# Optimization experiments

Measured on AMD Instinct MI355X. Metric: run time of the kernel, lower is better.

Reference implementation:

```python
import jax, jax.numpy as jnp
import numpy as np

# --- model constants (from init_kwargs) ---
COUNT = 8          # number of layer stacks (king buckets)
L1 = 3072          # input feature dim (2*L1//2 == L1)
L2 = 15            # first hidden dim per stack (l1 outputs L2+1: L2 hidden + 1 skip)
L3 = 32            # second hidden dim per stack
SQ_CORR = 127.0 / 128.0   # sqcrele_correction_factor
MAX_ACT = 1.0             # max_hidden_activation (clipped ReLU ceiling)
BATCH = 32768


def setup_inputs() -> dict:
    key = jax.random.key(0)
    ks = jax.random.split(key, 8)
    x = jax.random.normal(ks[0], (BATCH, L1), dtype=jnp.float32)
    routing_data = jax.random.randint(ks[1], (BATCH,), 0, COUNT, dtype=jnp.int64)
    # StackedLinear weights: [count, out_features, in_features]
    w1 = jax.random.normal(ks[2], (COUNT, L2 + 1, L1), dtype=jnp.float32) * 0.01
    b1 = jax.random.normal(ks[3], (COUNT, L2 + 1), dtype=jnp.float32) * 0.01
    w2 = jax.random.normal(ks[4], (COUNT, L3, 2 * L2), dtype=jnp.float32) * 0.05
    b2 = jax.random.normal(ks[5], (COUNT, L3), dtype=jnp.float32) * 0.01
    w3 = jax.random.normal(ks[6], (COUNT, 1, L3), dtype=jnp.float32) * 0.05
    b3 = jnp.zeros((COUNT, 1), dtype=jnp.float32)  # output bias zeroed in __init__
    return {"x": x, "routing_data": routing_data,
            "w1": w1, "b1": b1, "w2": w2, "b2": b2, "w3": w3, "b3": b3}


def reference(x, routing_data, w1, b1, w2, b2, w3, b3):
    # l1: apply all COUNT linears to the shared input -> [B, count, L2+1]
    l1c = jnp.einsum('bi,coi->bco', x, w1) + b1
    l1x, l1x_out = l1c[..., :L2], l1c[..., L2:]            # [B,c,L2], [B,c,1]
    sqr_l1x = (l1x * l1x) * SQ_CORR
    h1 = jnp.clip(jnp.concatenate([sqr_l1x, l1x], axis=2), 0.0, MAX_ACT)  # [B,c,2*L2]
    # l2: per-stack linear -> [B, count, L3]
    h2 = jnp.clip(jnp.einsum('bci,coi->bco', h1, w2) + b2, 0.0, MAX_ACT)
    # output: per-stack linear -> [B, count, 1], plus skip connection
    l3x = jnp.einsum('bci,coi->bco', h2, w3) + b3 + l1x_out
    # hard-index routing: gather the selected stack per batch element -> [B, 1]
    idx = routing_data.astype(jnp.int32)[:, None, None]
    return jnp.take_along_axis(l3x, idx, axis=1).squeeze(1)
```

## Files before the change

### kernel.cpp

```cpp
#include <hip/hip_runtime.h>

#define NEXP   8
#define L1DIM  3072
#define BATCH  32768
#define SQCORR (127.0f / 128.0f)
#define CHUNK  256
#define NCHUNK (L1DIM / CHUNK)

#define CUR_STRIDE  16
#define WS_CURSORS  0
#define WS_SORTED   (NEXP * CUR_STRIDE)
#define NBLK_SORT   (BATCH / 256)
#define BLK_PER_E   (BATCH / 16)
#define NBLK_MAIN   (NEXP * BLK_PER_E)

__global__ void init_k(int* ws) {
    if (threadIdx.x < NEXP)
        ws[WS_CURSORS + threadIdx.x * CUR_STRIDE] = threadIdx.x * BATCH;
}

__global__ void scatter_k(const int* __restrict__ routing, int* ws) {
    __shared__ int h[NEXP];
    __shared__ int base[NEXP];
    if (threadIdx.x < NEXP) h[threadIdx.x] = 0;
    __syncthreads();
    int i = blockIdx.x * 256 + threadIdx.x;
    int e = routing[i];
    int rank = atomicAdd(&h[e], 1);
    __syncthreads();
    if (threadIdx.x < NEXP)
        base[threadIdx.x] =
            atomicAdd(&ws[WS_CURSORS + threadIdx.x * CUR_STRIDE], h[threadIdx.x]);
    __syncthreads();
    ws[WS_SORTED + base[e] + rank] = i;
}

__device__ __forceinline__ void lds_cp16(void* lds, const void* g) {
    __builtin_amdgcn_global_load_lds(
        (const __attribute__((address_space(1))) void*)g,
        (__attribute__((address_space(3))) void*)lds, 16, 0, 0);
}

__global__ __launch_bounds__(256, 3) void moe_main_k(
        const float* __restrict__ x, const int* __restrict__ ws,
        const float* __restrict__ w1, const float* __restrict__ b1,
        const float* __restrict__ w2, const float* __restrict__ b2,
        const float* __restrict__ w3, const float* __restrict__ b3,
        float* __restrict__ out) {
    __shared__ float xs[3][16][CHUNK];
    __shared__ float tot[4][64];

    const int e   = blockIdx.x % NEXP;
    const int b16 = (blockIdx.x / NEXP) * 16;
    const int n   = ws[WS_CURSORS + e * CUR_STRIDE] - e * BATCH;
    if (b16 >= n) return;

    const int tid  = threadIdx.x;
    const int wid  = tid >> 6;
    const int lane = tid & 63;
    const int r0   = wid * 4;
    const int loff = lane * 4;

    int rows[4];
    const float* xp[4];
    #pragma unroll
    for (int q = 0; q < 4; ++q) {
        int s = b16 + r0 + q;
        rows[q] = (s < n) ? ws[WS_SORTED + e * BATCH + s] : -1;
        int r = rows[q] < 0 ? 0 : rows[q];
        xp[q] = x + (size_t)r * L1DIM;
    }
    const float* w1e = w1 + (size_t)e * 16 * L1DIM;

    auto issue_x = [&](int t, int b) {
        const int koff = t * CHUNK + loff;
        #pragma unroll
        for (int q = 0; q < 4; ++q)
            lds_cp16(&xs[b][r0 + q][loff], xp[q] + koff);
    };

    float acc[64];
    #pragma unroll
    for (int k = 0; k < 64; ++k) acc[k] = 0.0f;

    issue_x(0, 0);
    issue_x(1, 1);

    #pragma unroll 1
    for (int t = 0; t < NCHUNK; ++t) {
        const int xb = t % 3;
        asm volatile("s_waitcnt vmcnt(4)" ::: "memory");

        float4 xv[4];
        #pragma unroll
        for (int q = 0; q < 4; ++q)
            xv[q] = *(const float4*)&xs[xb][r0 + q][loff];

        const float* wc = w1e + t * CHUNK + loff;
        float4 wv[16];
        #pragma unroll
        for (int o = 0; o < 16; ++o)
            wv[o] = *(const float4*)(wc + (size_t)o * L1DIM);

        __builtin_amdgcn_sched_barrier(0);
        if (t + 2 < NCHUNK) issue_x(t + 2, (t + 2) % 3);
        __builtin_amdgcn_sched_barrier(0);

        #pragma unroll
        for (int o = 0; o < 16; ++o) {
            #pragma unroll
            for (int q = 0; q < 4; ++q) {
                float s = acc[q * 16 + o];
                s = fmaf(xv[q].x, wv[o].x, s);
                s = fmaf(xv[q].y, wv[o].y, s);
                s = fmaf(xv[q].z, wv[o].z, s);
                s = fmaf(xv[q].w, wv[o].w, s);
                acc[q * 16 + o] = s;
            }
        }
    }

    #pragma unroll
    for (int s = 0; s < 6; ++s) {
        const int mask = 32 >> s;
        const bool hi = (lane & mask) != 0;
        #pragma unroll
        for (int k = 0; k < 32; ++k) {
            if (k >= mask) break;
            float give = hi ? acc[k] : acc[k + mask];
            float got  = __shfl_xor(give, mask, 64);
            float keep = hi ? acc[k + mask] : acc[k];
            acc[k] = keep + got;
        }
    }

    tot[wid][lane] = acc[0];
    __syncthreads();

    const int q = lane >> 4;
    const int j = lane & 15;
    const int row = rows[q];

    const float* tq = &tot[wid][q * 16];
    float l1x_out = tq[15] + b1[e * 16 + 15];

    float h1v[30];
    #pragma unroll
    for (int i = 0; i < 15; ++i) {
        float t = tq[i] + b1[e * 16 + i];
        float sq = t * t * SQCORR;
        h1v[i]      = fminf(fmaxf(sq, 0.0f), 1.0f);
        h1v[i + 15] = fminf(fmaxf(t,  0.0f), 1.0f);
    }

    float s0 = b2[e * 32 + j];
    float s1 = b2[e * 32 + 16 + j];
    const float* w2e = w2 + (size_t)e * 32 * 30;
    #pragma unroll
    for (int i = 0; i < 30; ++i) {
        s0 = fmaf(h1v[i], w2e[j * 30 + i], s0);
        s1 = fmaf(h1v[i], w2e[(16 + j) * 30 + i], s1);
    }
    s0 = fminf(fmaxf(s0, 0.0f), 1.0f);
    s1 = fminf(fmaxf(s1, 0.0f), 1.0f);

    float p = s0 * w3[e * 32 + j] + s1 * w3[e * 32 + 16 + j];
    #pragma unroll
    for (int m = 8; m >= 1; m >>= 1) p += __shfl_xor(p, m, 64);

    if (j == 0 && row >= 0) out[row] = p + b3[e] + l1x_out;
}

extern "C" void kernel_launch(void* const* d_in, const int* in_sizes, int n_in,
                              void* d_out, int out_size, void* d_ws, size_t ws_size,
                              hipStream_t stream) {
    const float* x       = (const float*)d_in[0];
    const int*   routing = (const int*)d_in[1];
    const float* w1      = (const float*)d_in[2];
    const float* b1      = (const float*)d_in[3];
    const float* w2      = (const float*)d_in[4];
    const float* b2      = (const float*)d_in[5];
    const float* w3      = (const float*)d_in[6];
    const float* b3      = (const float*)d_in[7];
    float* out = (float*)d_out;
    int*   ws  = (int*)d_ws;

    init_k<<<1, 64, 0, stream>>>(ws);
    scatter_k<<<NBLK_SORT, 256, 0, stream>>>(routing, ws);
    moe_main_k<<<NBLK_MAIN, 256, 0, stream>>>(x, ws, w1, b1, w2, b2, w3, b3, out);
}
```

Measured before the change: 137.8 us.

## Split W1 outputs across waves and share all 16 x rows via LDS

Each wave now loads only its 4 of the 16 W1 output rows per chunk, instead of all 16, and computes those outputs for all 16 batch rows read from shared LDS. A block barrier is added each iteration so that every wave's x loads are visible. The final cross-wave reduction gathers the per-row results from the tot array. This cuts per-wave global weight traffic and register pressure fourfold, at the cost of more LDS reads, a barrier per chunk, and a lower occupancy hint (2 instead of 3).

```diff
diff --git a/kernel.cpp b/kernel.cpp
--- a/kernel.cpp
+++ b/kernel.cpp
@@ -41,7 +41,7 @@
         (__attribute__((address_space(3))) void*)lds, 16, 0, 0);
 }
 
-__global__ __launch_bounds__(256, 3) void moe_main_k(
+__global__ __launch_bounds__(256, 2) void moe_main_k(
         const float* __restrict__ x, const int* __restrict__ ws,
         const float* __restrict__ w1, const float* __restrict__ b1,
         const float* __restrict__ w2, const float* __restrict__ b2,
@@ -70,9 +70,10 @@
         int r = rows[q] < 0 ? 0 : rows[q];
         xp[q] = x + (size_t)r * L1DIM;
     }
-    const float* w1e = w1 + (size_t)e * 16 * L1DIM;
-
-    auto issue_x = [&](int t, int b) {
+    const float* w1e = w1 + ((size_t)e * 16 + wid * 4) * L1DIM + loff;
+
+    auto issue_x = [&](int t) {
+        const int b = t % 3;
         const int koff = t * CHUNK + loff;
         #pragma unroll
         for (int q = 0; q < 4; ++q)
@@ -83,39 +84,43 @@
     #pragma unroll
     for (int k = 0; k < 64; ++k) acc[k] = 0.0f;
 
-    issue_x(0, 0);
-    issue_x(1, 1);
+    issue_x(0);
+    issue_x(1);
 
     #pragma unroll 1
     for (int t = 0; t < NCHUNK; ++t) {
         const int xb = t % 3;
         asm volatile("s_waitcnt vmcnt(4)" ::: "memory");
-
-        float4 xv[4];
-        #pragma unroll
-        for (int q = 0; q < 4; ++q)
-            xv[q] = *(const float4*)&xs[xb][r0 + q][loff];
-
-        const float* wc = w1e + t * CHUNK + loff;
-        float4 wv[16];
-        #pragma unroll
-        for (int o = 0; o < 16; ++o)
-            wv[o] = *(const float4*)(wc + (size_t)o * L1DIM);
-
+        __builtin_amdgcn_s_barrier();
         __builtin_amdgcn_sched_barrier(0);
-        if (t + 2 < NCHUNK) issue_x(t + 2, (t + 2) % 3);
+
+        float4 wv[4];
+        #pragma unroll
+        for (int oo = 0; oo < 4; ++oo)
+            wv[oo] = *(const float4*)(w1e + t * CHUNK + (size_t)oo * L1DIM);
+
         __builtin_amdgcn_sched_barrier(0);
-
-        #pragma unroll
-        for (int o = 0; o < 16; ++o) {
+        if (t + 2 < NCHUNK) issue_x(t + 2);
+        __builtin_amdgcn_sched_barrier(0);
+
+        #pragma unroll
+        for (int rg = 0; rg < 4; ++rg) {
+            float4 xv[4];
             #pragma unroll
-            for (int q = 0; q < 4; ++q) {
-                float s = acc[q * 16 + o];
-                s = fmaf(xv[q].x, wv[o].x, s);
-                s = fmaf(xv[q].y, wv[o].y, s);
-                s = fmaf(xv[q].z, wv[o].z, s);
-                s = fmaf(xv[q].w, wv[o].w, s);
-                acc[q * 16 + o] = s;
+            for (int rr = 0; rr < 4; ++rr)
+                xv[rr] = *(const float4*)&xs[xb][rg * 4 + rr][loff];
+            #pragma unroll
+            for (int oo = 0; oo < 4; ++oo) {
+                #pragma unroll
+                for (int rr = 0; rr < 4; ++rr) {
+                    const int v = (rg * 4 + rr) * 4 + oo;
+                    float a = acc[v];
+                    a = fmaf(xv[rr].x, wv[oo].x, a);
+                    a = fmaf(xv[rr].y, wv[oo].y, a);
+                    a = fmaf(xv[rr].z, wv[oo].z, a);
+                    a = fmaf(xv[rr].w, wv[oo].w, a);
+                    acc[v] = a;
+                }
             }
         }
     }
@@ -140,17 +145,22 @@
     const int q = lane >> 4;
     const int j = lane & 15;
     const int row = rows[q];
-
-    const float* tq = &tot[wid][q * 16];
+    const int rl  = wid * 4 + q;
+
+    float tq[16];
+    #pragma unroll
+    for (int i = 0; i < 16; ++i)
+        tq[i] = tot[i >> 2][rl * 4 + (i & 3)];
+
     float l1x_out = tq[15] + b1[e * 16 + 15];
 
     float h1v[30];
     #pragma unroll
     for (int i = 0; i < 15; ++i) {
-        float t = tq[i] + b1[e * 16 + i];
-        float sq = t * t * SQCORR;
+        float v = tq[i] + b1[e * 16 + i];
+        float sq = v * v * SQCORR;
         h1v[i]      = fminf(fmaxf(sq, 0.0f), 1.0f);
-        h1v[i + 15] = fminf(fmaxf(t,  0.0f), 1.0f);
+        h1v[i + 15] = fminf(fmaxf(v,  0.0f), 1.0f);
     }
 
     float s0 = b2[e * 32 + j];
```

Result: faster. 112.0 us (-18.7%).
